# Performance work log

Measured on AMD Instinct MI355X. Metric: run time of the kernel, lower is better.

The kernel has to match this reference:

```python
import jax, jax.numpy as jnp
import numpy as np

H = 16          # num attention heads (== num kv heads here)
D = 128         # head_dim
HID = 2048      # hidden_size = H * D
THETA = 10000.0
SCALE = 1.0 / (D ** 0.5)
EPS = 1e-8


def rotate_half(x):
    x1, x2 = x[..., : D // 2], x[..., D // 2 :]
    return jnp.concatenate((-x2, x1), axis=-1)


def rope_tables(seq_len):
    inv_freq = 1.0 / (THETA ** (jnp.arange(0, D, 2, dtype=jnp.float32) / D))
    freqs = jnp.outer(jnp.arange(seq_len, dtype=jnp.float32), inv_freq)  # [S, D/2]
    emb = jnp.concatenate((freqs, freqs), axis=-1)                        # [S, D]
    return jnp.cos(emb), jnp.sin(emb)


def setup_inputs() -> dict:
    key = jax.random.key(0)
    ks = jax.random.split(key, 10)
    B, S = 1, 2048
    hidden_states = jax.random.normal(ks[0], (B, S, HID), jnp.float32) * 0.02
    position_ids = jnp.tile(jnp.arange(S, dtype=jnp.int32)[None, :], (B, 1))
    # additive causal mask, shape (B, 1, S, S) as asserted in the torch forward
    causal = jnp.tril(jnp.ones((S, S), dtype=bool))
    attention_mask = jnp.where(causal, 0.0, -1e9).astype(jnp.float32)[None, None]
    attention_mask = jnp.tile(attention_mask, (B, 1, 1, 1))
    Wq = jax.random.normal(ks[1], (HID, HID), jnp.float32) * 0.02
    bq = jax.random.normal(ks[2], (HID,), jnp.float32) * 0.02
    Wk = jax.random.normal(ks[3], (HID, HID), jnp.float32) * 0.02
    bk = jax.random.normal(ks[4], (HID,), jnp.float32) * 0.02
    Wo = jax.random.normal(ks[5], (HID, HID), jnp.float32) * 0.02
    beta = jax.random.normal(ks[6], (1,), jnp.float32)
    M = jax.random.normal(ks[7], (H, D, D), jnp.float32) * 0.02
    z = jax.random.uniform(ks[8], (H, D), jnp.float32) * 100.0 + 1.0  # positive accumulator
    return {
        "hidden_states": hidden_states,
        "attention_mask": attention_mask,
        "position_ids": position_ids,
        "Wq": Wq, "bq": bq, "Wk": Wk, "bk": bk, "Wo": Wo,
        "beta": beta, "M": M, "z": z,
    }


def reference(hidden_states, attention_mask, position_ids, Wq, bq, Wk, bk, Wo, beta, M, z):
    B, S, _ = hidden_states.shape
    # projections (NOTE: source uses q_proj for value_states too -- reproduced faithfully)
    q = (hidden_states @ Wq + bq).reshape(B, S, H, D).transpose(0, 2, 1, 3)  # [B,H,S,D]
    k = (hidden_states @ Wk + bk).reshape(B, S, H, D).transpose(0, 2, 1, 3)
    v = q  # value_states = q_proj(hidden_states), no RoPE applied to values

    cos, sin = rope_tables(S)
    cos = cos[position_ids][:, None]  # [B,1,S,D]
    sin = sin[position_ids][:, None]
    qr = q * cos + rotate_half(q) * sin
    kr = k * cos + rotate_half(k) * sin

    # --- compressive memory retrieval (with pre-update M, z) ---
    sq = jax.nn.elu(qr) + 1.0                                  # [B,H,S,D]
    mem_num = jnp.einsum('bhsd,hde->bhse', sq, M)              # [B,H,S,D]
    mem_den = jnp.einsum('bhsd,hd->bhs', sq, z)[..., None] + EPS
    memory_output = mem_num / mem_den

    # --- memory update: outer-product accumulation ---
    sk = jax.nn.elu(kr) + 1.0
    M_new = M + jnp.einsum('bhsd,bhse->hde', sk, v)
    z_new = z + sk.sum(axis=(0, 2))

    # --- local attention (SDPA with additive mask, dropout 0) ---
    scores = jnp.einsum('bhsd,bhtd->bhst', qr, kr) * SCALE + attention_mask
    probs = jax.nn.softmax(scores, axis=-1)
    attn_output = jnp.einsum('bhst,bhtd->bhsd', probs, v)

    # --- long-term memory injection: sigmoid-gated blend ---
    g = jax.nn.sigmoid(beta)[0]
    combined = g * memory_output + (1.0 - g) * attn_output     # [B,H,S,D]
    combined = combined.transpose(0, 2, 1, 3).reshape(B, S, HID)
    final_output = combined @ Wo
    return (final_output, M_new, z_new)
```

## Files before the change

kernel.cpp:

```cpp
#include <hip/hip_runtime.h>
#include <hip/hip_bf16.h>


#define S_LEN 2048
#define HID 2048
#define NH 16
#define HD 128
#define SCALE_QK 0.088388347648318447f

typedef __attribute__((ext_vector_type(8))) short bf16x8;
typedef __attribute__((ext_vector_type(4))) float f32x4;

__device__ __forceinline__ short f2bf(float f) {
  __hip_bfloat16 h = __float2bfloat16(f);
  return __builtin_bit_cast(short, h);
}
__device__ __forceinline__ float bf2f(short s) {
  unsigned int u = ((unsigned int)(unsigned short)s) << 16;
  return __builtin_bit_cast(float, u);
}
__device__ __forceinline__ void gload16(const void* g, void* l) {
  __builtin_amdgcn_global_load_lds(
      (const __attribute__((address_space(1))) void*)g,
      (__attribute__((address_space(3))) void*)l, 16, 0, 0);
}

__global__ __launch_bounds__(256) void f32_to_bf16_kernel(
    const float* __restrict__ in, short* __restrict__ out) {
  size_t i = (size_t)(blockIdx.x * 256 + threadIdx.x) * 8;
  float4 a = *reinterpret_cast<const float4*>(in + i);
  float4 b = *reinterpret_cast<const float4*>(in + i + 4);
  alignas(16) short t[8] = {f2bf(a.x), f2bf(a.y), f2bf(a.z), f2bf(a.w),
                            f2bf(b.x), f2bf(b.y), f2bf(b.z), f2bf(b.w)};
  *reinterpret_cast<int4*>(out + i) = *reinterpret_cast<int4*>(t);
}

__global__ __launch_bounds__(256) void transpose_f2b_kernel(
    const float* __restrict__ in, short* __restrict__ out, int R, int C) {
  __shared__ float t[32][33];
  size_t bo = (size_t)blockIdx.z * R * C;
  int r0 = blockIdx.y * 32, c0 = blockIdx.x * 32;
  int tx = threadIdx.x & 31, ty = threadIdx.x >> 5;
#pragma unroll
  for (int i = 0; i < 4; ++i)
    t[ty + i * 8][tx] = in[bo + (size_t)(r0 + ty + i * 8) * C + c0 + tx];
  __syncthreads();
#pragma unroll
  for (int i = 0; i < 4; ++i)
    out[bo + (size_t)(c0 + ty + i * 8) * R + r0 + tx] = f2bf(t[tx][ty + i * 8]);
}

__global__ __launch_bounds__(256) void transpose_b2b_kernel(
    const short* __restrict__ in, short* __restrict__ out, int R, int C) {
  __shared__ short t[32][33];
  int r0 = blockIdx.y * 32, c0 = blockIdx.x * 32;
  int tx = threadIdx.x & 31, ty = threadIdx.x >> 5;
#pragma unroll
  for (int i = 0; i < 4; ++i)
    t[ty + i * 8][tx] = in[(size_t)(r0 + ty + i * 8) * C + c0 + tx];
  __syncthreads();
#pragma unroll
  for (int i = 0; i < 4; ++i)
    out[(size_t)(c0 + ty + i * 8) * R + r0 + tx] = t[tx][ty + i * 8];
}

__global__ __launch_bounds__(256) void tables_kernel(
    const int* __restrict__ pos_ids, float* __restrict__ cost,
    float* __restrict__ sint) {
  int idx = blockIdx.x * 256 + threadIdx.x;
  int s = idx >> 6, j = idx & 63;
  float pos = (float)pos_ids[s];
  float inv = powf(10000.0f, -((float)j) / 64.0f);
  float a = pos * inv;
  cost[idx] = cosf(a);
  sint[idx] = sinf(a);
}

__global__ __launch_bounds__(256) void gemm_bt_dual_kernel(
    const short* __restrict__ A, const short* __restrict__ BT,
    const float* __restrict__ bias0, const float* __restrict__ bias1,
    float* __restrict__ C0, float* __restrict__ C1) {
  __shared__ short As[128 * 64];
  __shared__ short Bs[128 * 64];
  const int K = 2048;
  const int tid = threadIdx.x;
  const int wave = tid >> 6, lane = tid & 63;
  const int g = lane >> 4, l15 = lane & 15;
  const int wm = (wave >> 1) * 64, wn = (wave & 1) * 64;
  const int row0 = blockIdx.x * 128;
  const int colg0 = blockIdx.y * 128;

  const int ld_r = wave * 32 + (lane >> 3);
  const int ld_c = (lane & 7) * 8;
  const short* Ag = A + (size_t)(row0 + ld_r) * K + ld_c;
  const short* Bg = BT + (size_t)(colg0 + ld_r) * K + ld_c;
  short* Al = As + wave * 2048;
  short* Bl = Bs + wave * 2048;

  f32x4 acc[4][4] = {};
  for (int kt = 0; kt < K; kt += 64) {
    __syncthreads();
#pragma unroll
    for (int i = 0; i < 4; ++i) {
      gload16(Ag + kt + (size_t)i * 8 * K, Al + i * 512);
      gload16(Bg + kt + (size_t)i * 8 * K, Bl + i * 512);
    }
    __syncthreads();
#pragma unroll
    for (int ks = 0; ks < 2; ++ks) {
      bf16x8 a[4], b[4];
#pragma unroll
      for (int m = 0; m < 4; ++m)
        a[m] = *reinterpret_cast<bf16x8*>(
            reinterpret_cast<char*>(As) + (wm + m * 16 + l15) * 128 +
            (ks * 32 + g * 8) * 2);
#pragma unroll
      for (int n = 0; n < 4; ++n)
        b[n] = *reinterpret_cast<bf16x8*>(
            reinterpret_cast<char*>(Bs) + (wn + n * 16 + l15) * 128 +
            (ks * 32 + g * 8) * 2);
#pragma unroll
      for (int m = 0; m < 4; ++m)
#pragma unroll
        for (int n = 0; n < 4; ++n)
          acc[m][n] = __builtin_amdgcn_mfma_f32_16x16x32_bf16(a[m], b[n],
                                                              acc[m][n], 0, 0, 0);
    }
  }

  float* C = (colg0 < 2048) ? C0 : C1;
  const float* bias = (colg0 < 2048) ? bias0 : bias1;
  const int col0 = (colg0 < 2048) ? colg0 : colg0 - 2048;
#pragma unroll
  for (int m = 0; m < 4; ++m)
#pragma unroll
    for (int n = 0; n < 4; ++n) {
      int row = row0 + wm + m * 16 + g * 4;
      int col = col0 + wn + n * 16 + l15;
      float bv = bias ? bias[col] : 0.0f;
#pragma unroll
      for (int r = 0; r < 4; ++r)
        C[(size_t)(row + r) * 2048 + col] = acc[m][n][r] + bv;
    }
}

__global__ __launch_bounds__(256) void rope_kernel(
    const float* __restrict__ qf, const float* __restrict__ kf,
    const float* __restrict__ cost, const float* __restrict__ sint,
    short* __restrict__ qr, short* __restrict__ kr, short* __restrict__ sq,
    short* __restrict__ sk, short* __restrict__ v) {
  int s = blockIdx.x;
  int hd = threadIdx.x * 8;
  int d = hd & 127;
  bool lo = d < 64;
  size_t base = (size_t)s * HID + hd;
  size_t pb = lo ? base + 64 : base - 64;
  int tb = s * 64 + (hd & 63);
  alignas(16) short oqr[8], okr[8], osq[8], osk[8], ov[8];
#pragma unroll
  for (int j = 0; j < 8; ++j) {
    float c = cost[tb + j], sn = sint[tb + j];
    float q = qf[base + j], qp = qf[pb + j];
    float k = kf[base + j], kp = kf[pb + j];
    float rq = lo ? -qp : qp;
    float rk = lo ? -kp : kp;
    float qrv = q * c + rq * sn;
    float krv = k * c + rk * sn;
    oqr[j] = f2bf(qrv);
    okr[j] = f2bf(krv);
    osq[j] = f2bf(qrv > 0.0f ? qrv + 1.0f : __expf(qrv));
    osk[j] = f2bf(krv > 0.0f ? krv + 1.0f : __expf(krv));
    ov[j] = f2bf(q);
  }
  *reinterpret_cast<int4*>(qr + base) = *reinterpret_cast<int4*>(oqr);
  *reinterpret_cast<int4*>(kr + base) = *reinterpret_cast<int4*>(okr);
  *reinterpret_cast<int4*>(sq + base) = *reinterpret_cast<int4*>(osq);
  *reinterpret_cast<int4*>(sk + base) = *reinterpret_cast<int4*>(osk);
  *reinterpret_cast<int4*>(v + base) = *reinterpret_cast<int4*>(ov);
}

__global__ __launch_bounds__(256) void attn_kernel(
    const short* __restrict__ qr, const short* __restrict__ kr,
    const short* __restrict__ vT, float* __restrict__ attn_out) {
  __shared__ short kr_s[128 * 128];
  __shared__ short vT_s[128 * 128];
  __shared__ short p_s[4][16 * 128];
  const int tid = threadIdx.x;
  const int wave = tid >> 6, lane = tid & 63;
  const int g = lane >> 4, l15 = lane & 15;
  const int bid = blockIdx.x;
  const int h = bid & 15;
  const int u = bid >> 4;
  const int qt = (u < 16) ? (2 * u) : (31 - 2 * (u - 16));
  const int q0 = qt * 64;
  const int ntiles = (qt >> 1) + 1;

  bf16x8 qf[4];
#pragma unroll
  for (int ks = 0; ks < 4; ++ks) {
    int row = q0 + wave * 16 + l15;
    qf[ks] = *reinterpret_cast<const bf16x8*>(qr + (size_t)row * HID + h * HD +
                                              ks * 32 + g * 8);
  }

  f32x4 o[8] = {};
  float m_run[4], l_run[4];
#pragma unroll
  for (int r = 0; r < 4; ++r) {
    m_run[r] = -3.0e38f;
    l_run[r] = 0.0f;
  }

  for (int kt = 0; kt < ntiles; ++kt) {
    const int t0 = kt * 128;
    __syncthreads();
#pragma unroll
    for (int i = 0; i < 8; ++i) {
      int c = tid + 256 * i;
      int r = c >> 4, kc = c & 15;
      int off = (r * 256 + kc * 16) ^ ((r & 7) << 4);
      *reinterpret_cast<int4*>(reinterpret_cast<char*>(kr_s) + off) =
          *reinterpret_cast<const int4*>(kr + (size_t)(t0 + r) * HID + h * HD +
                                         kc * 8);
      *reinterpret_cast<int4*>(reinterpret_cast<char*>(vT_s) + off) =
          *reinterpret_cast<const int4*>(vT + (size_t)(h * HD + r) * S_LEN + t0 +
                                         kc * 8);
    }
    __syncthreads();

    f32x4 sfr[8] = {};
#pragma unroll
    for (int n = 0; n < 8; ++n) {
#pragma unroll
      for (int ks = 0; ks < 4; ++ks) {
        int rr = n * 16 + l15;
        int off = (rr * 256 + (ks * 32 + g * 8) * 2) ^ ((rr & 7) << 4);
        bf16x8 b =
            *reinterpret_cast<bf16x8*>(reinterpret_cast<char*>(kr_s) + off);
        sfr[n] = __builtin_amdgcn_mfma_f32_16x16x32_bf16(qf[ks], b, sfr[n], 0,
                                                         0, 0);
      }
    }

#pragma unroll
    for (int r = 0; r < 4; ++r) {
      const int srow = q0 + wave * 16 + g * 4 + r;
      float mx = m_run[r];
#pragma unroll
      for (int n = 0; n < 8; ++n) {
        int t = t0 + n * 16 + l15;
        float val = sfr[n][r] * SCALE_QK;
        val = (t <= srow) ? val : -3.0e38f;
        sfr[n][r] = val;
        mx = fmaxf(mx, val);
      }
      mx = fmaxf(mx, __shfl_xor(mx, 1));
      mx = fmaxf(mx, __shfl_xor(mx, 2));
      mx = fmaxf(mx, __shfl_xor(mx, 4));
      mx = fmaxf(mx, __shfl_xor(mx, 8));
      float sum = 0.0f;
#pragma unroll
      for (int n = 0; n < 8; ++n) {
        float p = __expf(sfr[n][r] - mx);
        sfr[n][r] = p;
        sum += p;
      }
      sum += __shfl_xor(sum, 1);
      sum += __shfl_xor(sum, 2);
      sum += __shfl_xor(sum, 4);
      sum += __shfl_xor(sum, 8);
      float f = __expf(m_run[r] - mx);
      l_run[r] = l_run[r] * f + sum;
      m_run[r] = mx;
#pragma unroll
      for (int n = 0; n < 8; ++n) o[n][r] *= f;
    }

    char* pw = reinterpret_cast<char*>(p_s[wave]);
#pragma unroll
    for (int n = 0; n < 8; ++n)
#pragma unroll
      for (int r = 0; r < 4; ++r) {
        int rl = g * 4 + r;
        int off = (rl * 256 + (n * 16 + l15) * 2) ^ ((rl & 7) << 4);
        *reinterpret_cast<short*>(pw + off) = f2bf(sfr[n][r]);
      }

#pragma unroll
    for (int ks = 0; ks < 4; ++ks) {
      int offp = (l15 * 256 + (ks * 32 + g * 8) * 2) ^ ((l15 & 7) << 4);
      bf16x8 pa = *reinterpret_cast<bf16x8*>(pw + offp);
#pragma unroll
      for (int n = 0; n < 8; ++n) {
        int rr = n * 16 + l15;
        int off = (rr * 256 + (ks * 32 + g * 8) * 2) ^ ((rr & 7) << 4);
        bf16x8 vb =
            *reinterpret_cast<bf16x8*>(reinterpret_cast<char*>(vT_s) + off);
        o[n] = __builtin_amdgcn_mfma_f32_16x16x32_bf16(pa, vb, o[n], 0, 0, 0);
      }
    }
  }

#pragma unroll
  for (int n = 0; n < 8; ++n)
#pragma unroll
    for (int r = 0; r < 4; ++r) {
      int row = q0 + wave * 16 + g * 4 + r;
      int col = n * 16 + l15;
      attn_out[(size_t)row * HID + h * HD + col] = o[n][r] / l_run[r];
    }
}

__global__ __launch_bounds__(256) void mem_combine_kernel(
    const short* __restrict__ sq, const short* __restrict__ MT,
    const float* __restrict__ z, const float* __restrict__ attn,
    const float* __restrict__ beta, short* __restrict__ combined) {
  __shared__ short mt_s[128 * 128];
  const int tid = threadIdx.x;
  const int wave = tid >> 6, lane = tid & 63;
  const int g = lane >> 4, l15 = lane & 15;
  const int h = blockIdx.y;
  const int s0 = blockIdx.x * 128;
#pragma unroll
  for (int i = 0; i < 8; ++i) {
    int c = tid + 256 * i;
    int r = c >> 4, kc = c & 15;
    int off = (r * 256 + kc * 16) ^ ((r & 7) << 4);
    *reinterpret_cast<int4*>(reinterpret_cast<char*>(mt_s) + off) =
        *reinterpret_cast<const int4*>(MT + (size_t)h * 16384 + r * 128 + kc * 8);
  }
  __syncthreads();

  f32x4 acc[2][8] = {};
#pragma unroll
  for (int ks = 0; ks < 4; ++ks) {
    bf16x8 a[2];
#pragma unroll
    for (int m = 0; m < 2; ++m) {
      int row = s0 + wave * 32 + m * 16 + l15;
      a[m] = *reinterpret_cast<const bf16x8*>(sq + (size_t)row * HID + h * HD +
                                              ks * 32 + g * 8);
    }
#pragma unroll
    for (int n = 0; n < 8; ++n) {
      int rr = n * 16 + l15;
      int off = (rr * 256 + (ks * 32 + g * 8) * 2) ^ ((rr & 7) << 4);
      bf16x8 b = *reinterpret_cast<bf16x8*>(reinterpret_cast<char*>(mt_s) + off);
#pragma unroll
      for (int m = 0; m < 2; ++m)
        acc[m][n] =
            __builtin_amdgcn_mfma_f32_16x16x32_bf16(a[m], b, acc[m][n], 0, 0, 0);
    }
  }

  float den[2][4];
#pragma unroll
  for (int m = 0; m < 2; ++m)
#pragma unroll
    for (int r = 0; r < 4; ++r) {
      int row = s0 + wave * 32 + m * 16 + g * 4 + r;
      bf16x8 sv = *reinterpret_cast<const bf16x8*>(sq + (size_t)row * HID +
                                                   h * HD + l15 * 8);
      float part = 0.0f;
#pragma unroll
      for (int j = 0; j < 8; ++j) part += bf2f(sv[j]) * z[h * HD + l15 * 8 + j];
      part += __shfl_xor(part, 1);
      part += __shfl_xor(part, 2);
      part += __shfl_xor(part, 4);
      part += __shfl_xor(part, 8);
      den[m][r] = part + 1e-8f;
    }
  float gv = 1.0f / (1.0f + expf(-beta[0]));
#pragma unroll
  for (int m = 0; m < 2; ++m)
#pragma unroll
    for (int n = 0; n < 8; ++n)
#pragma unroll
      for (int r = 0; r < 4; ++r) {
        int row = s0 + wave * 32 + m * 16 + g * 4 + r;
        int col = n * 16 + l15;
        float mem = acc[m][n][r] / den[m][r];
        float at = attn[(size_t)row * HID + h * HD + col];
        combined[(size_t)row * HID + h * HD + col] =
            f2bf(gv * mem + (1.0f - gv) * at);
      }
}

__global__ __launch_bounds__(256) void mnew_part_kernel(
    const short* __restrict__ skT, const short* __restrict__ vT,
    float* __restrict__ part) {
  const int sp = blockIdx.x;
  const int h = blockIdx.y;
  const int tid = threadIdx.x;
  const int wave = tid >> 6, lane = tid & 63;
  const int g = lane >> 4, l15 = lane & 15;
  f32x4 acc[2][8] = {};
  for (int ks = sp * 8; ks < sp * 8 + 8; ++ks) {
    bf16x8 a[2];
#pragma unroll
    for (int m = 0; m < 2; ++m) {
      int dd = wave * 32 + m * 16 + l15;
      a[m] = *reinterpret_cast<const bf16x8*>(skT + (size_t)(h * HD + dd) * S_LEN +
                                              ks * 32 + g * 8);
    }
#pragma unroll
    for (int n = 0; n < 8; ++n) {
      int e = n * 16 + l15;
      bf16x8 b = *reinterpret_cast<const bf16x8*>(
          vT + (size_t)(h * HD + e) * S_LEN + ks * 32 + g * 8);
#pragma unroll
      for (int m = 0; m < 2; ++m)
        acc[m][n] =
            __builtin_amdgcn_mfma_f32_16x16x32_bf16(a[m], b, acc[m][n], 0, 0, 0);
    }
  }
#pragma unroll
  for (int m = 0; m < 2; ++m)
#pragma unroll
    for (int n = 0; n < 8; ++n)
#pragma unroll
      for (int r = 0; r < 4; ++r) {
        int dd = wave * 32 + m * 16 + g * 4 + r;
        int e = n * 16 + l15;
        part[(size_t)(sp * 16 + h) * 16384 + (size_t)dd * 128 + e] =
            acc[m][n][r];
      }
}

__global__ __launch_bounds__(256) void mnew_reduce_kernel(
    const float* __restrict__ part, const float* __restrict__ Mold,
    float* __restrict__ Mout) {
  int idx = blockIdx.x * 256 + threadIdx.x;
  int j4 = idx * 4;
  int h = j4 >> 14;
  int rem = j4 & 16383;
  float4 a = *reinterpret_cast<const float4*>(Mold + j4);
#pragma unroll
  for (int s = 0; s < 8; ++s) {
    float4 p = *reinterpret_cast<const float4*>(
        part + ((size_t)(s * 16 + h) << 14) + rem);
    a.x += p.x;
    a.y += p.y;
    a.z += p.z;
    a.w += p.w;
  }
  *reinterpret_cast<float4*>(Mout + j4) = a;
}

__global__ __launch_bounds__(256) void znew_kernel(const short* __restrict__ skT,
                                                   const float* __restrict__ z,
                                                   float* __restrict__ out) {
  int row = blockIdx.x;
  int tid = threadIdx.x;
  bf16x8 vv = *reinterpret_cast<const bf16x8*>(skT + (size_t)row * S_LEN + tid * 8);
  float s = 0.0f;
#pragma unroll
  for (int j = 0; j < 8; ++j) s += bf2f(vv[j]);
#pragma unroll
  for (int off = 1; off < 64; off <<= 1) s += __shfl_xor(s, off);
  __shared__ float wsum[4];
  if ((tid & 63) == 0) wsum[tid >> 6] = s;
  __syncthreads();
  if (tid == 0) out[row] = z[row] + wsum[0] + wsum[1] + wsum[2] + wsum[3];
}

extern "C" void kernel_launch(void* const* d_in, const int* in_sizes, int n_in,
                              void* d_out, int out_size, void* d_ws,
                              size_t ws_size, hipStream_t stream) {
  const float* hs = (const float*)d_in[0];
  const int* pos = (const int*)d_in[2];
  const float* Wq = (const float*)d_in[3];
  const float* bq = (const float*)d_in[4];
  const float* Wk = (const float*)d_in[5];
  const float* bk = (const float*)d_in[6];
  const float* Wo = (const float*)d_in[7];
  const float* beta = (const float*)d_in[8];
  const float* Mm = (const float*)d_in[9];
  const float* z = (const float*)d_in[10];
  float* out = (float*)d_out;

  char* ws = (char*)d_ws;
  const size_t MB = 1u << 20;
  float* q_f32 = (float*)(ws + 0);
  float* k_f32 = (float*)(ws + 16 * MB);
  short* hs_b = (short*)(ws + 32 * MB);
  short* WqkT = (short*)(ws + 40 * MB);
  short* WoT = (short*)(ws + 56 * MB);
  short* qr = (short*)(ws + 64 * MB);
  short* kr = (short*)(ws + 72 * MB);
  short* sq = (short*)(ws + 80 * MB);
  short* vT = (short*)(ws + 88 * MB);
  short* MT = (short*)(ws + 96 * MB);
  float* cost = (float*)(ws + 96 * MB + 512 * 1024);
  float* sint = (float*)(ws + 97 * MB);
  float* attn = q_f32;
  short* comb = (short*)k_f32;
  short* sk = hs_b;
  short* v = WqkT;
  short* skT = WqkT + 4 * 1024 * 1024;
  float* mpart = q_f32;

  f32_to_bf16_kernel<<<2048, 256, 0, stream>>>(hs, hs_b);
  transpose_f2b_kernel<<<dim3(64, 64, 1), 256, 0, stream>>>(Wq, WqkT, 2048, 2048);
  transpose_f2b_kernel<<<dim3(64, 64, 1), 256, 0, stream>>>(
      Wk, WqkT + 4 * 1024 * 1024, 2048, 2048);
  transpose_f2b_kernel<<<dim3(64, 64, 1), 256, 0, stream>>>(Wo, WoT, 2048, 2048);
  transpose_f2b_kernel<<<dim3(4, 4, 16), 256, 0, stream>>>(Mm, MT, 128, 128);
  tables_kernel<<<512, 256, 0, stream>>>(pos, cost, sint);

  gemm_bt_dual_kernel<<<dim3(16, 32), 256, 0, stream>>>(hs_b, WqkT, bq, bk,
                                                        q_f32, k_f32);
  rope_kernel<<<2048, 256, 0, stream>>>(q_f32, k_f32, cost, sint, qr, kr, sq, sk,
                                        v);
  transpose_b2b_kernel<<<dim3(64, 64, 1), 256, 0, stream>>>(v, vT, 2048, 2048);
  transpose_b2b_kernel<<<dim3(64, 64, 1), 256, 0, stream>>>(sk, skT, 2048, 2048);

  attn_kernel<<<512, 256, 0, stream>>>(qr, kr, vT, attn);
  mem_combine_kernel<<<dim3(16, 16), 256, 0, stream>>>(sq, MT, z, attn, beta,
                                                       comb);
  gemm_bt_dual_kernel<<<dim3(16, 16), 256, 0, stream>>>(comb, WoT, nullptr,
                                                        nullptr, out, out);
  mnew_part_kernel<<<dim3(8, 16), 256, 0, stream>>>(skT, vT, mpart);
  mnew_reduce_kernel<<<256, 256, 0, stream>>>(mpart, Mm, out + 4194304);
  znew_kernel<<<2048, 256, 0, stream>>>(skT, z, out + 4194304 + 16 * 128 * 128);
}
```

Before: 442.9 us.

## Fuse memory-retrieval combine into attention kernel with double-buffered 64-key tiles

The attention kernel now walks 64-key tiles instead of 128, so the causal loop does less wasted work on the diagonal and applies the mask only on the diagonal tile. The next K/V tile is prefetched into registers and written to a second LDS buffer while the current tile is computed, which overlaps global loads with MFMA work. The memory-retrieval matmul, denominator and sigmoid blend are folded into the attention epilogue, which removes a separate launch and the fp32 round-trip of the attention output. In exchange there are more loop iterations with softmax reductions, and register pressure rises from the prefetch registers.

```diff
diff --git a/kernel.cpp b/kernel.cpp
--- a/kernel.cpp
+++ b/kernel.cpp
@@ -181,10 +181,12 @@
 
 __global__ __launch_bounds__(256) void attn_kernel(
     const short* __restrict__ qr, const short* __restrict__ kr,
-    const short* __restrict__ vT, float* __restrict__ attn_out) {
-  __shared__ short kr_s[128 * 128];
-  __shared__ short vT_s[128 * 128];
-  __shared__ short p_s[4][16 * 128];
+    const short* __restrict__ vT, const short* __restrict__ sq,
+    const short* __restrict__ MT, const float* __restrict__ z,
+    const float* __restrict__ beta, short* __restrict__ comb) {
+  __shared__ short k_s[2][64 * 128];
+  __shared__ short v_s[2][128 * 64];
+  __shared__ short p_s[4][16 * 64];
   const int tid = threadIdx.x;
   const int wave = tid >> 6, lane = tid & 63;
   const int g = lane >> 4, l15 = lane & 15;
@@ -193,7 +195,7 @@
   const int u = bid >> 4;
   const int qt = (u < 16) ? (2 * u) : (31 - 2 * (u - 16));
   const int q0 = qt * 64;
-  const int ntiles = (qt >> 1) + 1;
+  const int ntiles = qt + 1;
 
   bf16x8 qf[4];
 #pragma unroll
@@ -203,6 +205,36 @@
                                               ks * 32 + g * 8);
   }
 
+  int4 kreg[4], vreg[4];
+#define LOAD_TILE(T0)                                                         \
+  {                                                                           \
+    _Pragma("unroll") for (int i = 0; i < 4; ++i) {                           \
+      int c = tid + 256 * i;                                                  \
+      kreg[i] = *reinterpret_cast<const int4*>(                               \
+          kr + (size_t)((T0) + (c >> 4)) * HID + h * HD + (c & 15) * 8);      \
+      vreg[i] = *reinterpret_cast<const int4*>(                               \
+          vT + (size_t)(h * HD + (c >> 3)) * S_LEN + (T0) + (c & 7) * 8);     \
+    }                                                                         \
+  }
+#define WRITE_TILE(B)                                                         \
+  {                                                                           \
+    _Pragma("unroll") for (int i = 0; i < 4; ++i) {                           \
+      int c = tid + 256 * i;                                                  \
+      int rk = c >> 4, ck = c & 15;                                           \
+      *reinterpret_cast<int4*>(reinterpret_cast<char*>(k_s[B]) +              \
+                               ((rk * 256 + ck * 16) ^ ((rk & 7) << 4))) =    \
+          kreg[i];                                                            \
+      int rv = c >> 3, cv = c & 7;                                            \
+      *reinterpret_cast<int4*>(reinterpret_cast<char*>(v_s[B]) +              \
+                               ((rv * 128 + cv * 16) ^ ((rv & 7) << 4))) =    \
+          vreg[i];                                                            \
+    }                                                                         \
+  }
+
+  LOAD_TILE(0);
+  WRITE_TILE(0);
+  __syncthreads();
+
   f32x4 o[8] = {};
   float m_run[4], l_run[4];
 #pragma unroll
@@ -212,45 +244,35 @@
   }
 
   for (int kt = 0; kt < ntiles; ++kt) {
-    const int t0 = kt * 128;
-    __syncthreads();
-#pragma unroll
-    for (int i = 0; i < 8; ++i) {
-      int c = tid + 256 * i;
-      int r = c >> 4, kc = c & 15;
-      int off = (r * 256 + kc * 16) ^ ((r & 7) << 4);
-      *reinterpret_cast<int4*>(reinterpret_cast<char*>(kr_s) + off) =
-          *reinterpret_cast<const int4*>(kr + (size_t)(t0 + r) * HID + h * HD +
-                                         kc * 8);
-      *reinterpret_cast<int4*>(reinterpret_cast<char*>(vT_s) + off) =
-          *reinterpret_cast<const int4*>(vT + (size_t)(h * HD + r) * S_LEN + t0 +
-                                         kc * 8);
-    }
-    __syncthreads();
-
-    f32x4 sfr[8] = {};
-#pragma unroll
-    for (int n = 0; n < 8; ++n) {
+    const int cur = kt & 1;
+    if (kt + 1 < ntiles) LOAD_TILE((kt + 1) * 64);
+
+    f32x4 sfr[4] = {};
+#pragma unroll
+    for (int n = 0; n < 4; ++n) {
 #pragma unroll
       for (int ks = 0; ks < 4; ++ks) {
         int rr = n * 16 + l15;
         int off = (rr * 256 + (ks * 32 + g * 8) * 2) ^ ((rr & 7) << 4);
         bf16x8 b =
-            *reinterpret_cast<bf16x8*>(reinterpret_cast<char*>(kr_s) + off);
+            *reinterpret_cast<bf16x8*>(reinterpret_cast<char*>(k_s[cur]) + off);
         sfr[n] = __builtin_amdgcn_mfma_f32_16x16x32_bf16(qf[ks], b, sfr[n], 0,
                                                          0, 0);
       }
     }
 
+    const bool diag = (kt == qt);
 #pragma unroll
     for (int r = 0; r < 4; ++r) {
       const int srow = q0 + wave * 16 + g * 4 + r;
       float mx = m_run[r];
 #pragma unroll
-      for (int n = 0; n < 8; ++n) {
-        int t = t0 + n * 16 + l15;
+      for (int n = 0; n < 4; ++n) {
         float val = sfr[n][r] * SCALE_QK;
-        val = (t <= srow) ? val : -3.0e38f;
+        if (diag) {
+          int t = kt * 64 + n * 16 + l15;
+          val = (t <= srow) ? val : -3.0e38f;
+        }
         sfr[n][r] = val;
         mx = fmaxf(mx, val);
       }
@@ -260,7 +282,7 @@
       mx = fmaxf(mx, __shfl_xor(mx, 8));
       float sum = 0.0f;
 #pragma unroll
-      for (int n = 0; n < 8; ++n) {
+      for (int n = 0; n < 4; ++n) {
         float p = __expf(sfr[n][r] - mx);
         sfr[n][r] = p;
         sum += p;
@@ -278,112 +300,95 @@
 
     char* pw = reinterpret_cast<char*>(p_s[wave]);
 #pragma unroll
-    for (int n = 0; n < 8; ++n)
+    for (int n = 0; n < 4; ++n)
 #pragma unroll
       for (int r = 0; r < 4; ++r) {
         int rl = g * 4 + r;
-        int off = (rl * 256 + (n * 16 + l15) * 2) ^ ((rl & 7) << 4);
+        int off = (rl * 128 + (n * 16 + l15) * 2) ^ ((rl & 7) << 4);
         *reinterpret_cast<short*>(pw + off) = f2bf(sfr[n][r]);
       }
 
 #pragma unroll
-    for (int ks = 0; ks < 4; ++ks) {
-      int offp = (l15 * 256 + (ks * 32 + g * 8) * 2) ^ ((l15 & 7) << 4);
+    for (int ks = 0; ks < 2; ++ks) {
+      int offp = (l15 * 128 + (ks * 32 + g * 8) * 2) ^ ((l15 & 7) << 4);
       bf16x8 pa = *reinterpret_cast<bf16x8*>(pw + offp);
 #pragma unroll
       for (int n = 0; n < 8; ++n) {
         int rr = n * 16 + l15;
-        int off = (rr * 256 + (ks * 32 + g * 8) * 2) ^ ((rr & 7) << 4);
+        int off = (rr * 128 + (ks * 32 + g * 8) * 2) ^ ((rr & 7) << 4);
         bf16x8 vb =
-            *reinterpret_cast<bf16x8*>(reinterpret_cast<char*>(vT_s) + off);
+            *reinterpret_cast<bf16x8*>(reinterpret_cast<char*>(v_s[cur]) + off);
         o[n] = __builtin_amdgcn_mfma_f32_16x16x32_bf16(pa, vb, o[n], 0, 0, 0);
       }
     }
-  }
-
+
+    if (kt + 1 < ntiles) WRITE_TILE(cur ^ 1);
+    __syncthreads();
+  }
+#undef LOAD_TILE
+#undef WRITE_TILE
+
+  short* mt_s = &k_s[0][0];
+#pragma unroll
+  for (int i = 0; i < 8; ++i) {
+    int c = tid + 256 * i;
+    int r = c >> 4, kc = c & 15;
+    int4 d = *reinterpret_cast<const int4*>(MT + (size_t)h * 16384 + r * 128 +
+                                            kc * 8);
+    *reinterpret_cast<int4*>(reinterpret_cast<char*>(mt_s) +
+                             ((r * 256 + kc * 16) ^ ((r & 7) << 4))) = d;
+  }
+  __syncthreads();
+
+  bf16x8 af[4];
+#pragma unroll
+  for (int ks = 0; ks < 4; ++ks) {
+    int row = q0 + wave * 16 + l15;
+    af[ks] = *reinterpret_cast<const bf16x8*>(sq + (size_t)row * HID + h * HD +
+                                              ks * 32 + g * 8);
+  }
+  f32x4 acc2[8] = {};
+#pragma unroll
+  for (int ks = 0; ks < 4; ++ks) {
+#pragma unroll
+    for (int n = 0; n < 8; ++n) {
+      int rr = n * 16 + l15;
+      int off = (rr * 256 + (ks * 32 + g * 8) * 2) ^ ((rr & 7) << 4);
+      bf16x8 b =
+          *reinterpret_cast<bf16x8*>(reinterpret_cast<char*>(mt_s) + off);
+      acc2[n] = __builtin_amdgcn_mfma_f32_16x16x32_bf16(af[ks], b, acc2[n], 0,
+                                                        0, 0);
+    }
+  }
+
+  float den[4];
+#pragma unroll
+  for (int r = 0; r < 4; ++r) {
+    int row = q0 + wave * 16 + g * 4 + r;
+    bf16x8 sv =
+        *reinterpret_cast<const bf16x8*>(sq + (size_t)row * HID + h * HD +
+                                         l15 * 8);
+    float part = 0.0f;
+#pragma unroll
+    for (int j = 0; j < 8; ++j) part += bf2f(sv[j]) * z[h * HD + l15 * 8 + j];
+    part += __shfl_xor(part, 1);
+    part += __shfl_xor(part, 2);
+    part += __shfl_xor(part, 4);
+    part += __shfl_xor(part, 8);
+    den[r] = part + 1e-8f;
+  }
+
+  float gv = 1.0f / (1.0f + __expf(-beta[0]));
 #pragma unroll
   for (int n = 0; n < 8; ++n)
 #pragma unroll
     for (int r = 0; r < 4; ++r) {
       int row = q0 + wave * 16 + g * 4 + r;
       int col = n * 16 + l15;
-      attn_out[(size_t)row * HID + h * HD + col] = o[n][r] / l_run[r];
-    }
-}
-
-__global__ __launch_bounds__(256) void mem_combine_kernel(
-    const short* __restrict__ sq, const short* __restrict__ MT,
-    const float* __restrict__ z, const float* __restrict__ attn,
-    const float* __restrict__ beta, short* __restrict__ combined) {
-  __shared__ short mt_s[128 * 128];
-  const int tid = threadIdx.x;
-  const int wave = tid >> 6, lane = tid & 63;
-  const int g = lane >> 4, l15 = lane & 15;
-  const int h = blockIdx.y;
-  const int s0 = blockIdx.x * 128;
-#pragma unroll
-  for (int i = 0; i < 8; ++i) {
-    int c = tid + 256 * i;
-    int r = c >> 4, kc = c & 15;
-    int off = (r * 256 + kc * 16) ^ ((r & 7) << 4);
-    *reinterpret_cast<int4*>(reinterpret_cast<char*>(mt_s) + off) =
-        *reinterpret_cast<const int4*>(MT + (size_t)h * 16384 + r * 128 + kc * 8);
-  }
-  __syncthreads();
-
-  f32x4 acc[2][8] = {};
-#pragma unroll
-  for (int ks = 0; ks < 4; ++ks) {
-    bf16x8 a[2];
-#pragma unroll
-    for (int m = 0; m < 2; ++m) {
-      int row = s0 + wave * 32 + m * 16 + l15;
-      a[m] = *reinterpret_cast<const bf16x8*>(sq + (size_t)row * HID + h * HD +
-                                              ks * 32 + g * 8);
-    }
-#pragma unroll
-    for (int n = 0; n < 8; ++n) {
-      int rr = n * 16 + l15;
-      int off = (rr * 256 + (ks * 32 + g * 8) * 2) ^ ((rr & 7) << 4);
-      bf16x8 b = *reinterpret_cast<bf16x8*>(reinterpret_cast<char*>(mt_s) + off);
-#pragma unroll
-      for (int m = 0; m < 2; ++m)
-        acc[m][n] =
-            __builtin_amdgcn_mfma_f32_16x16x32_bf16(a[m], b, acc[m][n], 0, 0, 0);
-    }
-  }
-
-  float den[2][4];
-#pragma unroll
-  for (int m = 0; m < 2; ++m)
-#pragma unroll
-    for (int r = 0; r < 4; ++r) {
-      int row = s0 + wave * 32 + m * 16 + g * 4 + r;
-      bf16x8 sv = *reinterpret_cast<const bf16x8*>(sq + (size_t)row * HID +
-                                                   h * HD + l15 * 8);
-      float part = 0.0f;
-#pragma unroll
-      for (int j = 0; j < 8; ++j) part += bf2f(sv[j]) * z[h * HD + l15 * 8 + j];
-      part += __shfl_xor(part, 1);
-      part += __shfl_xor(part, 2);
-      part += __shfl_xor(part, 4);
-      part += __shfl_xor(part, 8);
-      den[m][r] = part + 1e-8f;
-    }
-  float gv = 1.0f / (1.0f + expf(-beta[0]));
-#pragma unroll
-  for (int m = 0; m < 2; ++m)
-#pragma unroll
-    for (int n = 0; n < 8; ++n)
-#pragma unroll
-      for (int r = 0; r < 4; ++r) {
-        int row = s0 + wave * 32 + m * 16 + g * 4 + r;
-        int col = n * 16 + l15;
-        float mem = acc[m][n][r] / den[m][r];
-        float at = attn[(size_t)row * HID + h * HD + col];
-        combined[(size_t)row * HID + h * HD + col] =
-            f2bf(gv * mem + (1.0f - gv) * at);
-      }
+      float mem = acc2[n][r] / den[r];
+      float at = o[n][r] / l_run[r];
+      comb[(size_t)row * HID + h * HD + col] = f2bf(gv * mem + (1.0f - gv) * at);
+    }
 }
 
 __global__ __launch_bounds__(256) void mnew_part_kernel(
@@ -493,7 +498,6 @@
   short* MT = (short*)(ws + 96 * MB);
   float* cost = (float*)(ws + 96 * MB + 512 * 1024);
   float* sint = (float*)(ws + 97 * MB);
-  float* attn = q_f32;
   short* comb = (short*)k_f32;
   short* sk = hs_b;
   short* v = WqkT;
@@ -515,9 +519,7 @@
   transpose_b2b_kernel<<<dim3(64, 64, 1), 256, 0, stream>>>(v, vT, 2048, 2048);
   transpose_b2b_kernel<<<dim3(64, 64, 1), 256, 0, stream>>>(sk, skT, 2048, 2048);
 
-  attn_kernel<<<512, 256, 0, stream>>>(qr, kr, vT, attn);
-  mem_combine_kernel<<<dim3(16, 16), 256, 0, stream>>>(sq, MT, z, attn, beta,
-                                                       comb);
+  attn_kernel<<<512, 256, 0, stream>>>(qr, kr, vT, sq, MT, z, beta, comb);
   gemm_bt_dual_kernel<<<dim3(16, 16), 256, 0, stream>>>(comb, WoT, nullptr,
                                                         nullptr, out, out);
   mnew_part_kernel<<<dim3(8, 16), 256, 0, stream>>>(skT, vT, mpart);
```

Result: faster. 410.0 us (-7.4%).
